# Kernel tuning notes

Measured on AMD Instinct MI355X. Metric: run time of the kernel, lower is better.

The kernel has to match this reference:

```python
import jax, jax.numpy as jnp
import numpy as np

MUL0, MUL1 = 64, 32          # 64x0e + 32x1e irreps_emb
D_FEAT = MUL0 + 3 * MUL1     # 160
N_T, N_Q, N_K = 64, 1024, 1024


def quat_apply(q, v):
    # q: (...,4) real-first (w,x,y,z); v: (...,3). Rotate v by q.
    w = q[..., :1]
    u = q[..., 1:]
    uv = jnp.cross(u, v)
    return v + 2.0 * (w * uv + jnp.cross(u, uv))


def split_irreps(f):
    # f: (..., 160) -> scalars (...,64), vectors (...,32,3)
    s = f[..., :MUL0]
    v = f[..., MUL0:].reshape(f.shape[:-1] + (MUL1, 3))
    return s, v


def dtp(a, b, Ws, Wv):
    # Depthwise tensor product restricted to l<=1 (SeparableFCTP analogue),
    # output irreps 1x0e + 32x1e, with SiLU activation on the scalar part.
    sa, va = split_irreps(a)
    sb, vb = split_irreps(b)
    # scalar paths: 0e*0e and 1e.1e (dot) -> 96 scalar channels
    scal = jnp.concatenate([sa * sb, jnp.einsum('...ci,...ci->...c', va, vb)], axis=-1)
    # vector paths: 0e*1e, 1e*0e, 1e x 1e (cross) -> 96 vector channels
    vec = jnp.concatenate(
        [sa[..., :MUL1, None] * vb, va * sb[..., :MUL1, None], jnp.cross(va, vb)], axis=-2)
    out_s = jax.nn.silu(scal @ Ws)                    # (...,1)
    out_v = jnp.einsum('...ci,co->...oi', vec, Wv)    # (...,32,3)
    return out_s, out_v


def get_key_features(points, key_coord, key_feat, W_key):
    # radius-style key lookup: nearest key node + smooth radial envelope + linear
    d2 = jnp.sum((points[:, None, :] - key_coord[None, :, :]) ** 2, axis=-1)  # (M, N_K)
    idx = jnp.argmin(d2, axis=-1)
    dist = jnp.sqrt(jnp.take_along_axis(d2, idx[:, None], axis=1)[:, 0])
    env = jnp.exp(-dist)[:, None]
    return (key_feat[idx] * env) @ W_key              # (M, 160)


def setup_inputs() -> dict:
    key = jax.random.key(0)
    ks = jax.random.split(key, 11)
    return {
        'T': jax.random.normal(ks[0], (N_T, 7), jnp.float32),
        'query_weight': jax.random.uniform(ks[1], (N_Q,), jnp.float32),
        'query_feature': jax.random.normal(ks[2], (N_Q, D_FEAT), jnp.float32),
        'query_coord': jax.random.normal(ks[3], (N_Q, 3), jnp.float32),
        'key_coord': jax.random.normal(ks[4], (N_K, 3), jnp.float32),
        'key_node_feature': jax.random.normal(ks[5], (N_K, D_FEAT), jnp.float32),
        'W_key': jax.random.normal(ks[6], (D_FEAT, D_FEAT), jnp.float32) / np.sqrt(D_FEAT),
        'Ws_lin': jax.random.normal(ks[7], (96, 1), jnp.float32) / np.sqrt(96.0),
        'Wv_lin': jax.random.normal(ks[8], (96, 32), jnp.float32) / np.sqrt(96.0),
        'Ws_ang': jax.random.normal(ks[9], (96, 1), jnp.float32) / np.sqrt(96.0),
        'Wv_ang': jax.random.normal(ks[10], (96, 32), jnp.float32) / np.sqrt(96.0),
    }


def reference(T, query_weight, query_feature, query_coord, key_coord,
              key_node_feature, W_key, Ws_lin, Wv_lin, Ws_ang, Wv_ang):
    n_t = T.shape[0]
    n_q = query_feature.shape[0]
    q = T[:, :4]
    q = q / jnp.linalg.norm(q, axis=-1, keepdims=True)
    X = T[:, 4:]
    # transform query coords by each pose: (N_T, N_Q, 3)
    qc_t = quat_apply(q[:, None, :], query_coord[None, :, :]) + X[:, None, :]
    # equivariant feature transform: scalars unchanged, vectors rotated
    s, v = split_irreps(query_feature)
    v_t = quat_apply(q[:, None, None, :], v[None])                    # (N_T,N_Q,32,3)
    qf_t = jnp.concatenate(
        [jnp.broadcast_to(s, (n_t,) + s.shape), v_t.reshape(n_t, n_q, 3 * MUL1)],
        axis=-1).reshape(n_t * n_q, D_FEAT)
    # key feature gather over the expanded N_T*N_Q batch
    kf = get_key_features(qc_t.reshape(-1, 3), key_coord, key_node_feature, W_key)
    # two tensor products; original drops leading scalar ([..., 1:])
    _, lin = dtp(qf_t, kf, Ws_lin, Wv_lin)
    _, ang = dtp(qf_t, kf, Ws_ang, Wv_ang)
    lin = lin.reshape(n_t, n_q, MUL1, 3).mean(axis=-2)
    ang = ang.reshape(n_t, n_q, MUL1, 3).mean(axis=-2)
    # rotate back into body frame
    qinv = q * jnp.array([1.0, -1.0, -1.0, -1.0], q.dtype)
    lin = quat_apply(qinv[:, None, :], lin)
    ang = quat_apply(qinv[:, None, :], ang)
    ang_orbital = jnp.cross(query_coord[None], lin)
    lin_vel = jnp.einsum('q,tqi->ti', query_weight, lin)
    ang_vel = jnp.einsum('q,tqi->ti', query_weight, ang_orbital + ang)
    return lin_vel, ang_vel
```

## Files before the change

kernel.cpp:

```cpp
#include <hip/hip_runtime.h>
#include <math.h>

#define NT 64
#define NQ 1024
#define NK 1024
#define WS_KW 0
#define WS_QF 131072
#define WS_WV 262144
#define WS_KP 262400

__launch_bounds__(256)
__global__ void prep_kernel(const float* __restrict__ qfeat,
                            const float* __restrict__ keyfeat,
                            const float* __restrict__ Wkey,
                            const float* __restrict__ WvL,
                            const float* __restrict__ WvA,
                            const float* __restrict__ kcoord,
                            float* __restrict__ ws,
                            float* __restrict__ out) {
  const int blk = blockIdx.x;
  const int tid = threadIdx.x;
  if (blk < 128) {
    const int g = blk * 256 + tid;
    const int r = g >> 5;
    const int c = g & 31;
    const float* kf = keyfeat + r * 160;
    const int c0 = 64 + 3 * c;
    float a0 = 0.f, a1 = 0.f, a2 = 0.f, a3 = 0.f;
#pragma unroll 4
    for (int k = 0; k < 160; ++k) {
      const float f = kf[k];
      const float* wr = Wkey + k * 160;
      a0 = fmaf(f, wr[c0 + 0], a0);
      a1 = fmaf(f, wr[c0 + 1], a1);
      a2 = fmaf(f, wr[c0 + 2], a2);
      a3 = fmaf(f, wr[c], a3);
    }
    reinterpret_cast<float4*>(ws + WS_KW)[g] = make_float4(a0, a1, a2, a3);
  } else if (blk < 256) {
    const int g = (blk - 128) * 256 + tid;
    const int p = g >> 5;
    const int c = g & 31;
    const float* q = qfeat + p * 160;
    float4 o = make_float4(q[64 + 3 * c], q[65 + 3 * c], q[66 + 3 * c], q[c]);
    reinterpret_cast<float4*>(ws + WS_QF)[c * 1024 + p] = o;
  } else {
    out[tid] = 0.f;
    if (tid < 128) out[256 + tid] = 0.f;
    float4* kp = reinterpret_cast<float4*>(ws + WS_KP);
#pragma unroll
    for (int j = 0; j < 4; ++j) {
      const int k = j * 256 + tid;
      kp[k] = make_float4(kcoord[k * 3 + 0], kcoord[k * 3 + 1], kcoord[k * 3 + 2], 0.f);
    }
    if (tid < 32) {
      const int c = tid;
      float m0 = 0.f, m1 = 0.f, m2 = 0.f, m3 = 0.f, m4 = 0.f, m5 = 0.f;
      for (int o = 0; o < 32; ++o) {
        m0 += WvL[c * 32 + o];
        m1 += WvL[(32 + c) * 32 + o];
        m2 += WvL[(64 + c) * 32 + o];
        m3 += WvA[c * 32 + o];
        m4 += WvA[(32 + c) * 32 + o];
        m5 += WvA[(64 + c) * 32 + o];
      }
      float* wv = ws + WS_WV + c * 8;
      const float s = 1.0f / 32.0f;
      wv[0] = m0 * s; wv[1] = m1 * s; wv[2] = m2 * s;
      wv[3] = m3 * s; wv[4] = m4 * s; wv[5] = m5 * s;
      wv[6] = 0.f; wv[7] = 0.f;
    }
  }
}

__launch_bounds__(256)
__global__ void main_kernel(const float* __restrict__ T,
                            const float* __restrict__ qweight,
                            const float* __restrict__ qcoord,
                            const float* __restrict__ ws,
                            float* __restrict__ out) {
  __shared__ float2 cand[4][64];
  __shared__ float red[4][8];
  const int tid  = threadIdx.x;
  const int lane = tid & 63;
  const int wu   = __builtin_amdgcn_readfirstlane(tid >> 6);
  const int t    = blockIdx.x >> 4;
  const int pg   = blockIdx.x & 15;

  const float* Tt = T + t * 7;
  float qw = Tt[0], qx = Tt[1], qy = Tt[2], qz = Tt[3];
  const float Xx = Tt[4], Xy = Tt[5], Xz = Tt[6];
  const float rn = rsqrtf(qw * qw + qx * qx + qy * qy + qz * qz);
  qw *= rn; qx *= rn; qy *= rn; qz *= rn;
  const float ix = -qx, iy = -qy, iz = -qz;

  const int pA = pg * 64 + lane;
  const float qax = qcoord[pA * 3 + 0];
  const float qay = qcoord[pA * 3 + 1];
  const float qaz = qcoord[pA * 3 + 2];
  const float uvx0 = qy * qaz - qz * qay;
  const float uvy0 = qz * qax - qx * qaz;
  const float uvz0 = qx * qay - qy * qax;
  const float qcx = qax + 2.0f * (qw * uvx0 + (qy * uvz0 - qz * uvy0)) + Xx;
  const float qcy = qay + 2.0f * (qw * uvy0 + (qz * uvx0 - qx * uvz0)) + Xy;
  const float qcz = qaz + 2.0f * (qw * uvz0 + (qx * uvy0 - qy * uvx0)) + Xz;

  const float4* kp = reinterpret_cast<const float4*>(ws + WS_KP);
  const int kbase = wu * 256;
  float mv0 = 1e30f, mv1 = 1e30f;
  int mi0 = 0, mi1 = 0;
#pragma unroll 8
  for (int m = 0; m < 256; m += 2) {
    const float4 K0 = kp[kbase + m];
    const float4 K1 = kp[kbase + m + 1];
    const float dx0 = qcx - K0.x, dy0 = qcy - K0.y, dz0 = qcz - K0.z;
    const float dx1 = qcx - K1.x, dy1 = qcy - K1.y, dz1 = qcz - K1.z;
    const float d0 = dx0 * dx0 + dy0 * dy0 + dz0 * dz0;
    const float d1 = dx1 * dx1 + dy1 * dy1 + dz1 * dz1;
    if (d0 < mv0) { mv0 = d0; mi0 = kbase + m; }
    if (d1 < mv1) { mv1 = d1; mi1 = kbase + m + 1; }
  }
  float mvA = mv0; int miA = mi0;
  if (mv1 < mvA || (mv1 == mvA && mi1 < miA)) { mvA = mv1; miA = mi1; }
  cand[wu][lane] = make_float2(mvA, __int_as_float(miA));
  __syncthreads();

  const int pF  = pg * 64 + (tid >> 2);
  const int sub = tid & 3;
  const float2 c0 = cand[sub][tid >> 2];
  float mv = c0.x; int mi = __float_as_int(c0.y);
#pragma unroll
  for (int msk = 1; msk <= 2; msk <<= 1) {
    const float vo = __shfl_xor(mv, msk);
    const int   io = __shfl_xor(mi, msk);
    if (vo < mv || (vo == mv && io < mi)) { mv = vo; mi = io; }
  }
  const int minidx = mi;
  const float env = expf(-sqrtf(mv));

  const float qpx = qcoord[pF * 3 + 0];
  const float qpy = qcoord[pF * 3 + 1];
  const float qpz = qcoord[pF * 3 + 2];

  const float4* kwrow = reinterpret_cast<const float4*>(ws + WS_KW) + minidx * 32;
  const float4* qfp   = reinterpret_cast<const float4*>(ws + WS_QF) + pF;
  const float* wv = ws + WS_WV;
  float lx = 0.f, ly = 0.f, lz = 0.f, ax = 0.f, ay = 0.f, az = 0.f;
#pragma unroll
  for (int jj = 0; jj < 8; ++jj) {
    const int c = 4 * jj + sub;
    const float4 B = kwrow[c];
    const float4 A = qfp[c * 1024];
    const float uvx = iy * B.z - iz * B.y;
    const float uvy = iz * B.x - ix * B.z;
    const float uvz = ix * B.y - iy * B.x;
    const float bx = B.x + 2.0f * (qw * uvx + (iy * uvz - iz * uvy));
    const float by = B.y + 2.0f * (qw * uvy + (iz * uvx - ix * uvz));
    const float bz = B.z + 2.0f * (qw * uvz + (ix * uvy - iy * uvx));
    const float crx = A.y * bz - A.z * by;
    const float cry = A.z * bx - A.x * bz;
    const float crz = A.x * by - A.y * bx;
    const float* w6 = wv + c * 8;
    const float a1L = w6[0] * A.w, a2L = w6[1] * B.w, w3L = w6[2];
    const float a1A = w6[3] * A.w, a2A = w6[4] * B.w, w3A = w6[5];
    lx = fmaf(a1L, bx, fmaf(a2L, A.x, fmaf(w3L, crx, lx)));
    ly = fmaf(a1L, by, fmaf(a2L, A.y, fmaf(w3L, cry, ly)));
    lz = fmaf(a1L, bz, fmaf(a2L, A.z, fmaf(w3L, crz, lz)));
    ax = fmaf(a1A, bx, fmaf(a2A, A.x, fmaf(w3A, crx, ax)));
    ay = fmaf(a1A, by, fmaf(a2A, A.y, fmaf(w3A, cry, ay)));
    az = fmaf(a1A, bz, fmaf(a2A, A.z, fmaf(w3A, crz, az)));
  }
#pragma unroll
  for (int msk = 1; msk <= 2; msk <<= 1) {
    lx += __shfl_xor(lx, msk); ly += __shfl_xor(ly, msk); lz += __shfl_xor(lz, msk);
    ax += __shfl_xor(ax, msk); ay += __shfl_xor(ay, msk); az += __shfl_xor(az, msk);
  }
  lx *= env; ly *= env; lz *= env;
  ax *= env; ay *= env; az *= env;

  const float wp = qweight[pF];
  const float ox = qpy * lz - qpz * ly;
  const float oy = qpz * lx - qpx * lz;
  const float oz = qpx * ly - qpy * lx;
  float r0 = wp * lx, r1 = wp * ly, r2 = wp * lz;
  float r3 = wp * (ox + ax), r4 = wp * (oy + ay), r5 = wp * (oz + az);

#pragma unroll
  for (int m = 32; m >= 1; m >>= 1) {
    r0 += __shfl_xor(r0, m);
    r1 += __shfl_xor(r1, m);
    r2 += __shfl_xor(r2, m);
    r3 += __shfl_xor(r3, m);
    r4 += __shfl_xor(r4, m);
    r5 += __shfl_xor(r5, m);
  }
  const int wave = tid >> 6;
  const int lane2 = tid & 63;
  if (lane2 == 0) {
    red[wave][0] = r0; red[wave][1] = r1; red[wave][2] = r2;
    red[wave][3] = r3; red[wave][4] = r4; red[wave][5] = r5;
  }
  __syncthreads();
  if (tid < 6) {
    const float s = red[0][tid] + red[1][tid] + red[2][tid] + red[3][tid];
    const int row = (tid < 3) ? (t * 3 + tid) : (192 + t * 3 + (tid - 3));
    atomicAdd(out + row, s * 0.25f);
  }
}

extern "C" void kernel_launch(void* const* d_in, const int* in_sizes, int n_in,
                              void* d_out, int out_size, void* d_ws, size_t ws_size,
                              hipStream_t stream) {
  const float* T   = (const float*)d_in[0];
  const float* qw  = (const float*)d_in[1];
  const float* qf  = (const float*)d_in[2];
  const float* qc  = (const float*)d_in[3];
  const float* kc  = (const float*)d_in[4];
  const float* kf  = (const float*)d_in[5];
  const float* Wk  = (const float*)d_in[6];
  const float* WvL = (const float*)d_in[8];
  const float* WvA = (const float*)d_in[10];
  float* out = (float*)d_out;
  float* ws  = (float*)d_ws;

  prep_kernel<<<257, 256, 0, stream>>>(qf, kf, Wk, WvL, WvA, kc, ws, out);
  main_kernel<<<1024, 256, 0, stream>>>(T, qw, qc, ws, out);
}
```

Before: 119.1 us.

## Stage keys in LDS and process two queries per lane in nearest-key search

Each block now copies all 1024 key coordinates into shared memory and handles 128 queries instead of 64. Every lane evaluates two queries against each key it loads, so each key fetch is reused twice. The feature stage now splits the 32 channels over 2 lanes instead of 4, and the final scale changes from 0.25 to 0.5 to match. The grid is halved to 512 blocks, which lowers parallelism and adds 16KB of LDS per block in exchange for fewer key loads per distance computed.

```diff
diff --git a/kernel.cpp b/kernel.cpp
--- a/kernel.cpp
+++ b/kernel.cpp
@@ -79,13 +79,20 @@
                             const float* __restrict__ qcoord,
                             const float* __restrict__ ws,
                             float* __restrict__ out) {
-  __shared__ float2 cand[4][64];
+  __shared__ float4 keys[1024];
+  __shared__ float2 cand[4][128];
   __shared__ float red[4][8];
   const int tid  = threadIdx.x;
   const int lane = tid & 63;
   const int wu   = __builtin_amdgcn_readfirstlane(tid >> 6);
-  const int t    = blockIdx.x >> 4;
-  const int pg   = blockIdx.x & 15;
+  const int t    = blockIdx.x >> 3;
+  const int pg   = blockIdx.x & 7;
+
+  {
+    const float4* kp = reinterpret_cast<const float4*>(ws + WS_KP);
+#pragma unroll
+    for (int j = 0; j < 4; ++j) keys[j * 256 + tid] = kp[j * 256 + tid];
+  }
 
   const float* Tt = T + t * 7;
   float qw = Tt[0], qx = Tt[1], qy = Tt[2], qz = Tt[3];
@@ -94,50 +101,56 @@
   qw *= rn; qx *= rn; qy *= rn; qz *= rn;
   const float ix = -qx, iy = -qy, iz = -qz;
 
-  const int pA = pg * 64 + lane;
-  const float qax = qcoord[pA * 3 + 0];
-  const float qay = qcoord[pA * 3 + 1];
-  const float qaz = qcoord[pA * 3 + 2];
-  const float uvx0 = qy * qaz - qz * qay;
-  const float uvy0 = qz * qax - qx * qaz;
-  const float uvz0 = qx * qay - qy * qax;
-  const float qcx = qax + 2.0f * (qw * uvx0 + (qy * uvz0 - qz * uvy0)) + Xx;
-  const float qcy = qay + 2.0f * (qw * uvy0 + (qz * uvx0 - qx * uvz0)) + Xy;
-  const float qcz = qaz + 2.0f * (qw * uvz0 + (qx * uvy0 - qy * uvx0)) + Xz;
-
-  const float4* kp = reinterpret_cast<const float4*>(ws + WS_KP);
+  const int qA = pg * 128 + lane;
+  const int qB = qA + 64;
+  const float qax = qcoord[qA * 3 + 0], qay = qcoord[qA * 3 + 1], qaz = qcoord[qA * 3 + 2];
+  const float qbx = qcoord[qB * 3 + 0], qby = qcoord[qB * 3 + 1], qbz = qcoord[qB * 3 + 2];
+  const float uax = qy * qaz - qz * qay, uay = qz * qax - qx * qaz, uaz = qx * qay - qy * qax;
+  const float qcax = qax + 2.0f * (qw * uax + (qy * uaz - qz * uay)) + Xx;
+  const float qcay = qay + 2.0f * (qw * uay + (qz * uax - qx * uaz)) + Xy;
+  const float qcaz = qaz + 2.0f * (qw * uaz + (qx * uay - qy * uax)) + Xz;
+  const float ubx = qy * qbz - qz * qby, uby = qz * qbx - qx * qbz, ubz = qx * qby - qy * qbx;
+  const float qcbx = qbx + 2.0f * (qw * ubx + (qy * ubz - qz * uby)) + Xx;
+  const float qcby = qby + 2.0f * (qw * uby + (qz * ubx - qx * ubz)) + Xy;
+  const float qcbz = qbz + 2.0f * (qw * ubz + (qx * uby - qy * ubx)) + Xz;
+
+  __syncthreads();
+
   const int kbase = wu * 256;
-  float mv0 = 1e30f, mv1 = 1e30f;
-  int mi0 = 0, mi1 = 0;
+  float mvA = 1e30f, mvB = 1e30f;
+  int miA = 0, miB = 0;
 #pragma unroll 8
-  for (int m = 0; m < 256; m += 2) {
-    const float4 K0 = kp[kbase + m];
-    const float4 K1 = kp[kbase + m + 1];
-    const float dx0 = qcx - K0.x, dy0 = qcy - K0.y, dz0 = qcz - K0.z;
-    const float dx1 = qcx - K1.x, dy1 = qcy - K1.y, dz1 = qcz - K1.z;
-    const float d0 = dx0 * dx0 + dy0 * dy0 + dz0 * dz0;
-    const float d1 = dx1 * dx1 + dy1 * dy1 + dz1 * dz1;
-    if (d0 < mv0) { mv0 = d0; mi0 = kbase + m; }
-    if (d1 < mv1) { mv1 = d1; mi1 = kbase + m + 1; }
-  }
-  float mvA = mv0; int miA = mi0;
-  if (mv1 < mvA || (mv1 == mvA && mi1 < miA)) { mvA = mv1; miA = mi1; }
-  cand[wu][lane] = make_float2(mvA, __int_as_float(miA));
+  for (int m = 0; m < 256; ++m) {
+    const float4 K = keys[kbase + m];
+    const float dax = qcax - K.x, day = qcay - K.y, daz = qcaz - K.z;
+    const float dbx = qcbx - K.x, dby = qcby - K.y, dbz = qcbz - K.z;
+    const float dA = dax * dax + day * day + daz * daz;
+    const float dB = dbx * dbx + dby * dby + dbz * dbz;
+    if (dA < mvA) { mvA = dA; miA = kbase + m; }
+    if (dB < mvB) { mvB = dB; miB = kbase + m; }
+  }
+  cand[wu][lane]      = make_float2(mvA, __int_as_float(miA));
+  cand[wu][64 + lane] = make_float2(mvB, __int_as_float(miB));
   __syncthreads();
 
-  const int pF  = pg * 64 + (tid >> 2);
-  const int sub = tid & 3;
-  const float2 c0 = cand[sub][tid >> 2];
-  float mv = c0.x; int mi = __float_as_int(c0.y);
-#pragma unroll
-  for (int msk = 1; msk <= 2; msk <<= 1) {
-    const float vo = __shfl_xor(mv, msk);
-    const int   io = __shfl_xor(mi, msk);
+  const int pl  = tid >> 1;
+  const int sub = tid & 1;
+  const float2 ca = cand[2 * sub][pl];
+  const float2 cb = cand[2 * sub + 1][pl];
+  float mv = ca.x; int mi = __float_as_int(ca.y);
+  {
+    const float vb2 = cb.x; const int ib2 = __float_as_int(cb.y);
+    if (vb2 < mv || (vb2 == mv && ib2 < mi)) { mv = vb2; mi = ib2; }
+  }
+  {
+    const float vo = __shfl_xor(mv, 1);
+    const int   io = __shfl_xor(mi, 1);
     if (vo < mv || (vo == mv && io < mi)) { mv = vo; mi = io; }
   }
   const int minidx = mi;
   const float env = expf(-sqrtf(mv));
 
+  const int pF = pg * 128 + pl;
   const float qpx = qcoord[pF * 3 + 0];
   const float qpy = qcoord[pF * 3 + 1];
   const float qpz = qcoord[pF * 3 + 2];
@@ -147,8 +160,8 @@
   const float* wv = ws + WS_WV;
   float lx = 0.f, ly = 0.f, lz = 0.f, ax = 0.f, ay = 0.f, az = 0.f;
 #pragma unroll
-  for (int jj = 0; jj < 8; ++jj) {
-    const int c = 4 * jj + sub;
+  for (int jj = 0; jj < 16; ++jj) {
+    const int c = 2 * jj + sub;
     const float4 B = kwrow[c];
     const float4 A = qfp[c * 1024];
     const float uvx = iy * B.z - iz * B.y;
@@ -170,11 +183,8 @@
     ay = fmaf(a1A, by, fmaf(a2A, A.y, fmaf(w3A, cry, ay)));
     az = fmaf(a1A, bz, fmaf(a2A, A.z, fmaf(w3A, crz, az)));
   }
-#pragma unroll
-  for (int msk = 1; msk <= 2; msk <<= 1) {
-    lx += __shfl_xor(lx, msk); ly += __shfl_xor(ly, msk); lz += __shfl_xor(lz, msk);
-    ax += __shfl_xor(ax, msk); ay += __shfl_xor(ay, msk); az += __shfl_xor(az, msk);
-  }
+  lx += __shfl_xor(lx, 1); ly += __shfl_xor(ly, 1); lz += __shfl_xor(lz, 1);
+  ax += __shfl_xor(ax, 1); ay += __shfl_xor(ay, 1); az += __shfl_xor(az, 1);
   lx *= env; ly *= env; lz *= env;
   ax *= env; ay *= env; az *= env;
 
@@ -194,17 +204,15 @@
     r4 += __shfl_xor(r4, m);
     r5 += __shfl_xor(r5, m);
   }
-  const int wave = tid >> 6;
-  const int lane2 = tid & 63;
-  if (lane2 == 0) {
-    red[wave][0] = r0; red[wave][1] = r1; red[wave][2] = r2;
-    red[wave][3] = r3; red[wave][4] = r4; red[wave][5] = r5;
+  if (lane == 0) {
+    red[wu][0] = r0; red[wu][1] = r1; red[wu][2] = r2;
+    red[wu][3] = r3; red[wu][4] = r4; red[wu][5] = r5;
   }
   __syncthreads();
   if (tid < 6) {
     const float s = red[0][tid] + red[1][tid] + red[2][tid] + red[3][tid];
     const int row = (tid < 3) ? (t * 3 + tid) : (192 + t * 3 + (tid - 3));
-    atomicAdd(out + row, s * 0.25f);
+    atomicAdd(out + row, s * 0.5f);
   }
 }
 
@@ -224,5 +232,5 @@
   float* ws  = (float*)d_ws;
 
   prep_kernel<<<257, 256, 0, stream>>>(qf, kf, Wk, WvL, WvA, kc, ws, out);
-  main_kernel<<<1024, 256, 0, stream>>>(T, qw, qc, ws, out);
+  main_kernel<<<512, 256, 0, stream>>>(T, qw, qc, ws, out);
 }
```

After: 107.1 us. -10.1%, faster.
